# Kernel optimization log

Measured on AMD Instinct MI355X. Metric: run time of the kernel, lower is better.

Reference implementation:

```python
import jax, jax.numpy as jnp
import numpy as np

N_NODES = 100000
N_EDGES = 1600000
N_RELS = 8
IN_F, HID_F, OUT_F = 64, 64, 32


def rgcn_conv(x, src, dst, etype, W, root, bias, num_nodes, num_rels):
    """PyG RGCNConv: out[i] = x[i]@root + bias + sum_r mean_{j in N_r(i)} x[j]@W_r."""
    E = src.shape[0]
    seg = dst * num_rels + etype  # combined (node, relation) segment id
    cnt = jax.ops.segment_sum(jnp.ones((E,), x.dtype), seg,
                              num_segments=num_nodes * num_rels)
    norm = 1.0 / jnp.maximum(cnt[seg], 1.0)  # per-edge 1/|N_r(dst)|
    h = jnp.einsum('ni,rio->rno', x, W)      # [R, N, O] relation-transformed feats
    msg = h[etype, src] * norm[:, None]      # gather per edge, normalize
    agg = jax.ops.segment_sum(msg, dst, num_segments=num_nodes)
    return agg + x @ root + bias


def setup_inputs() -> dict:
    key = jax.random.key(0)
    ks = jax.random.split(key, 10)
    x = jax.random.normal(ks[0], (N_NODES, IN_F), dtype=jnp.float32)
    edge_index = jax.random.randint(ks[1], (2, N_EDGES), 0, N_NODES, dtype=jnp.int64)
    edge_type = jax.random.randint(ks[2], (N_EDGES,), 0, N_RELS, dtype=jnp.int64)
    s1 = 1.0 / np.sqrt(IN_F)
    s2 = 1.0 / np.sqrt(HID_F)
    W1 = jax.random.uniform(ks[3], (N_RELS, IN_F, HID_F), jnp.float32, -s1, s1)
    root1 = jax.random.uniform(ks[4], (IN_F, HID_F), jnp.float32, -s1, s1)
    b1 = jnp.zeros((HID_F,), jnp.float32)
    W2 = jax.random.uniform(ks[5], (N_RELS, HID_F, OUT_F), jnp.float32, -s2, s2)
    root2 = jax.random.uniform(ks[6], (HID_F, OUT_F), jnp.float32, -s2, s2)
    b2 = jnp.zeros((OUT_F,), jnp.float32)
    return {"x": x, "edge_index": edge_index, "edge_type": edge_type,
            "W1": W1, "root1": root1, "b1": b1,
            "W2": W2, "root2": root2, "b2": b2}


def reference(x, edge_index, edge_type, W1, root1, b1, W2, root2, b2):
    src, dst = edge_index[0], edge_index[1]
    h = rgcn_conv(x, src, dst, edge_type, W1, root1, b1, N_NODES, N_RELS)
    h = jax.nn.relu(h)
    out = rgcn_conv(h, src, dst, edge_type, W2, root2, b2, N_NODES, N_RELS)
    return out
```

## Files before the change

kernel.cpp:

```cpp
#include <hip/hip_runtime.h>
#include <hip/hip_bf16.h>

#define N_NODES 100000
#define N_EDGES 1600000
#define N_RELS  8
#define IN_F    64
#define HID_F   64
#define OUT_F   32
#define NSEG    (N_NODES * N_RELS)
#define SCAN_EPB 1024
#define SCAN_NB  ((NSEG + SCAN_EPB - 1) / SCAN_EPB)

typedef __attribute__((ext_vector_type(8))) short short8;
typedef __attribute__((ext_vector_type(4))) float f32x4;

__device__ __forceinline__ float b2f(unsigned short u) {
    return __uint_as_float(((unsigned)u) << 16);
}
__device__ __forceinline__ unsigned short f2b(float f) {
    unsigned u = __float_as_uint(f);
    u += 0x7FFFu + ((u >> 16) & 1u);
    return (unsigned short)(u >> 16);
}

#define PREP_W1 (576 * 64)
#define PREP_W2 (576 * 32)
#define PREP_CVT (N_NODES * 64 / 4)
#define PREP_TOT (PREP_W1 + PREP_W2 + PREP_CVT)

__global__ void k_hist(const int* __restrict__ dst, const int* __restrict__ et,
                       int* __restrict__ cnt, int* __restrict__ rank,
                       const float* __restrict__ W1, const float* __restrict__ root1,
                       const float* __restrict__ W2, const float* __restrict__ root2,
                       const float* __restrict__ x,
                       ushort* __restrict__ Wt1b, ushort* __restrict__ Wt2b,
                       ushort* __restrict__ xb) {
    const int e = blockIdx.x * 256 + threadIdx.x;
    const int gsz = gridDim.x * 256;
    for (int j = e; j < PREP_TOT; j += gsz) {
        if (j < PREP_W1) {
            int o = j / 576, k = j - o * 576;
            float v = (k < 512) ? W1[k * 64 + o] : root1[(k - 512) * 64 + o];
            Wt1b[j] = f2b(v);
        } else if (j < PREP_W1 + PREP_W2) {
            int j2 = j - PREP_W1;
            int o = j2 / 576, k = j2 - o * 576;
            float v = (k < 512) ? W2[k * 32 + o] : root2[(k - 512) * 32 + o];
            Wt2b[j2] = f2b(v);
        } else {
            int j2 = j - PREP_W1 - PREP_W2;
            float4 v = *(const float4*)(x + (size_t)j2 * 4);
            ushort4 u;
            u.x = f2b(v.x); u.y = f2b(v.y); u.z = f2b(v.z); u.w = f2b(v.w);
            *(ushort4*)(xb + (size_t)j2 * 4) = u;
        }
    }
    if (e < N_EDGES) {
        int seg = dst[e] * N_RELS + et[e];
        rank[e] = atomicAdd(&cnt[seg], 1);
    }
}

__global__ void k_scanA(const int* __restrict__ cnt, int* __restrict__ bsums) {
    __shared__ int red[256];
    int t = threadIdx.x;
    int base = blockIdx.x * SCAN_EPB + t * 4;
    int s = 0;
    #pragma unroll
    for (int j = 0; j < 4; ++j) {
        int idx = base + j;
        if (idx < NSEG) s += cnt[idx];
    }
    red[t] = s;
    __syncthreads();
    for (int st = 128; st > 0; st >>= 1) {
        if (t < st) red[t] += red[t + st];
        __syncthreads();
    }
    if (t == 0) bsums[blockIdx.x] = red[0];
}

__global__ void k_scanC(const int* __restrict__ cnt, const int* __restrict__ bsums,
                        int* __restrict__ offs) {
    __shared__ int red[256];
    __shared__ int ts[256];
    int t = threadIdx.x;

    int partial = 0;
    #pragma unroll
    for (int jj = 0; jj < 4; ++jj) {
        int j = t + jj * 256;
        if (j < SCAN_NB && j < (int)blockIdx.x) partial += bsums[j];
    }
    red[t] = partial;
    __syncthreads();
    for (int st = 128; st > 0; st >>= 1) {
        if (t < st) red[t] += red[t + st];
        __syncthreads();
    }
    const int base0 = red[0];

    int base = blockIdx.x * SCAN_EPB + t * 4;
    int v[4];
    int local = 0;
    #pragma unroll
    for (int j = 0; j < 4; ++j) {
        int idx = base + j;
        v[j] = (idx < NSEG) ? cnt[idx] : 0;
        local += v[j];
    }
    ts[t] = local;
    __syncthreads();
    for (int off = 1; off < 256; off <<= 1) {
        int x = (t >= off) ? ts[t - off] : 0;
        __syncthreads();
        ts[t] += x;
        __syncthreads();
    }
    int run = base0 + (ts[t] - local);
    #pragma unroll
    for (int j = 0; j < 4; ++j) {
        int idx = base + j;
        if (idx < NSEG) offs[idx] = run;
        run += v[j];
    }
}

__global__ void k_scat(const int* __restrict__ src, const int* __restrict__ dst,
                       const int* __restrict__ et, const int* __restrict__ offs,
                       const int* __restrict__ rank, int* __restrict__ ssrc) {
    int e = blockIdx.x * 256 + threadIdx.x;
    if (e < N_EDGES) {
        int r = et[e];
        int seg = dst[e] * N_RELS + r;
        ssrc[offs[seg] + rank[e]] = src[e] * 16 + r;
    }
}

template <int NOUT, bool RELU, typename OutT>
__global__ __launch_bounds__(512, 4) void k_layer(
        const ushort* __restrict__ xb, const int* __restrict__ offs,
        const int* __restrict__ cnt, const int* __restrict__ ssrc,
        const ushort* __restrict__ Wtb, const float* __restrict__ bias,
        OutT* __restrict__ out) {
    constexpr int NT = NOUT / 16;
    constexpr int S  = 8 / NT;
    __shared__ __align__(16) ushort A_lds[16][584];
    __shared__ f32x4 pc[6][64];

    const int tid = threadIdx.x;
    const int w = tid >> 6;
    const int f = tid & 63;
    const int node0 = blockIdx.x * 16;

    const int t = w % NT, q = w / NT;
    constexpr int cbase = 18 / S, crem = 18 % S;
    const int cs = q * cbase + (q < crem ? q : crem);
    const int ce = cs + cbase + (q < crem ? 1 : 0);
    const int n0 = t * 16;
    const ushort* bptr = Wtb + (n0 + (f & 15)) * 576 + ((f >> 4) * 8);
    short8 bcur = *(const short8*)(bptr + cs * 32);

    int ov = 0, cv = 0;
    if (f < 16) {
        ov = offs[(node0 + w * 2) * N_RELS + f];
        cv = cnt [(node0 + w * 2) * N_RELS + f];
    }

    for (int nd = 0; nd < 2; ++nd) {
        const int m = w * 2 + nd;
        const int node = node0 + m;
        const int s0 = __builtin_amdgcn_readlane(ov, nd * 8);
        const int ct = __builtin_amdgcn_readlane(ov, nd * 8 + 7)
                     + __builtin_amdgcn_readlane(cv, nd * 8 + 7) - s0;

        float a[8];
        #pragma unroll
        for (int r = 0; r < 8; ++r) a[r] = 0.0f;

        for (int cb = 0; cb < ct; cb += 64) {
            int n = ct - cb;
            if (n > 64) n = 64;
            int pk = 15;
            if (f < n) pk = ssrc[s0 + cb + f];
            for (int e = 0; e < n; e += 16) {
                int pv[16];
                float xv[16];
                #pragma unroll
                for (int i = 0; i < 16; ++i)
                    pv[i] = __builtin_amdgcn_readlane(pk, e + i);
                #pragma unroll
                for (int i = 0; i < 16; ++i)
                    xv[i] = b2f(xb[(size_t)(pv[i] >> 4) * 64 + f]);
                #pragma unroll
                for (int i = 0; i < 16; ++i) {
                    const int rl = pv[i] & 15;
                    if (rl < 4) {
                        if (rl < 2) { if (rl == 0) a[0] += xv[i]; else a[1] += xv[i]; }
                        else        { if (rl == 2) a[2] += xv[i]; else a[3] += xv[i]; }
                    } else if (rl < 8) {
                        if (rl < 6) { if (rl == 4) a[4] += xv[i]; else a[5] += xv[i]; }
                        else        { if (rl == 6) a[6] += xv[i]; else a[7] += xv[i]; }
                    }
                }
            }
        }

        #pragma unroll
        for (int r = 0; r < 8; ++r) {
            int c = __builtin_amdgcn_readlane(cv, nd * 8 + r);
            float inv = 1.0f / (float)(c > 0 ? c : 1);
            A_lds[m][r * 64 + f] = f2b(a[r] * inv);
        }
        A_lds[m][512 + f] = xb[node * 64 + f];
    }
    __syncthreads();

    f32x4 acc = (f32x4){0.0f, 0.0f, 0.0f, 0.0f};
    const ushort* aptr = &A_lds[f & 15][(f >> 4) * 8];
    for (int c = cs; c < ce; ++c) {
        short8 bnext = bcur;
        if (c + 1 < ce) bnext = *(const short8*)(bptr + (c + 1) * 32);
        short8 af = *(const short8*)(aptr + c * 32);
        acc = __builtin_amdgcn_mfma_f32_16x16x32_bf16(af, bcur, acc, 0, 0, 0);
        bcur = bnext;
    }

    if (q > 0) pc[w - NT][f] = acc;
    __syncthreads();
    if (q == 0) {
        #pragma unroll
        for (int j = 1; j < S; ++j) {
            f32x4 p = pc[t + NT * (j - 1)][f];
            acc.x += p.x; acc.y += p.y; acc.z += p.z; acc.w += p.w;
        }
        const int col = f & 15;
        const float bs = bias[n0 + col];
        const int mrow = (f >> 4) * 4;
        #pragma unroll
        for (int i = 0; i < 4; ++i) {
            float v = acc[i] + bs;
            if (RELU) v = fmaxf(v, 0.0f);
            size_t oi = (size_t)(node0 + mrow + i) * NOUT + n0 + col;
            if constexpr (sizeof(OutT) == 2) out[oi] = (OutT)f2b(v);
            else                             out[oi] = (OutT)v;
        }
    }
}

extern "C" void kernel_launch(void* const* d_in, const int* in_sizes, int n_in,
                              void* d_out, int out_size, void* d_ws, size_t ws_size,
                              hipStream_t stream) {
    const float* x     = (const float*)d_in[0];
    const int*   ei    = (const int*)d_in[1];
    const int*   et    = (const int*)d_in[2];
    const float* W1    = (const float*)d_in[3];
    const float* root1 = (const float*)d_in[4];
    const float* b1    = (const float*)d_in[5];
    const float* W2    = (const float*)d_in[6];
    const float* root2 = (const float*)d_in[7];
    const float* b2    = (const float*)d_in[8];
    float* out = (float*)d_out;

    const int* src = ei;
    const int* dst = ei + N_EDGES;

    char* ws = (char*)d_ws;
    int*    cnt   = (int*)(ws);
    int*    offs  = (int*)(ws + (size_t)NSEG * 4);
    int*    bsums = (int*)(ws + (size_t)NSEG * 8);
    int*    ssrc  = (int*)(ws + (size_t)NSEG * 8 + 4096);
    ushort* xb    = (ushort*)(ws + (size_t)NSEG * 8 + 4096 + (size_t)N_EDGES * 4);
    ushort* h1b   = (ushort*)((char*)xb + (size_t)N_NODES * 64 * 2);
    int*    rank  = (int*)h1b;
    ushort* Wt1b  = (ushort*)((char*)h1b + (size_t)N_NODES * 64 * 2);
    ushort* Wt2b  = (ushort*)((char*)Wt1b + (size_t)PREP_W1 * 2);

    hipMemsetAsync(cnt, 0, (size_t)NSEG * 4, stream);

    int eb = (N_EDGES + 255) / 256;
    k_hist<<<eb, 256, 0, stream>>>(dst, et, cnt, rank,
                                   W1, root1, W2, root2, x, Wt1b, Wt2b, xb);
    k_scanA<<<SCAN_NB, 256, 0, stream>>>(cnt, bsums);
    k_scanC<<<SCAN_NB, 256, 0, stream>>>(cnt, bsums, offs);
    k_scat<<<eb, 256, 0, stream>>>(src, dst, et, offs, rank, ssrc);

    k_layer<64, true, ushort><<<N_NODES / 16, 512, 0, stream>>>(
        xb, offs, cnt, ssrc, Wt1b, b1, h1b);
    k_layer<32, false, float><<<N_NODES / 16, 512, 0, stream>>>(
        h1b, offs, cnt, ssrc, Wt2b, b2, out);
}
```

Before: 438.7 us.

## Balance edge gather across waves via LDS atomics and scalar-loaded edge lists

Before this change each wave walked the edges of two fixed nodes, so the work per wave depended on node degree. Now the 16-node block's contiguous edge range is split evenly across the 8 waves. Each wave fetches 16 packed edge ids at a time with a scalar s_load_dwordx16, gathers source features, and accumulates them with LDS float atomicAdd into a 128x64 fp32 buffer indexed by (local node, relation), which is now packed into each edge id. The fp32 sums are then normalized, converted to bf16 and written back into the shared buffer before the MFMA stage. This removes the degree imbalance and the branchy per-relation register selection, at the cost of LDS atomic contention, extra barriers and larger shared memory that may lower occupancy.

Result: slower. 1.300 ms (+196.3%).

```diff
diff --git a/kernel.cpp b/kernel.cpp
--- a/kernel.cpp
+++ b/kernel.cpp
@@ -13,6 +13,7 @@
 
 typedef __attribute__((ext_vector_type(8))) short short8;
 typedef __attribute__((ext_vector_type(4))) float f32x4;
+typedef __attribute__((ext_vector_type(16))) int int16v;
 
 __device__ __forceinline__ float b2f(unsigned short u) {
     return __uint_as_float(((unsigned)u) << 16);
@@ -21,6 +22,12 @@
     unsigned u = __float_as_uint(f);
     u += 0x7FFFu + ((u >> 16) & 1u);
     return (unsigned short)(u >> 16);
+}
+__device__ __forceinline__ unsigned long long uni_ptr(const void* p) {
+    unsigned long long up = (unsigned long long)p;
+    unsigned lo = __builtin_amdgcn_readfirstlane((unsigned)up);
+    unsigned hi = __builtin_amdgcn_readfirstlane((unsigned)(up >> 32));
+    return ((unsigned long long)hi << 32) | lo;
 }
 
 #define PREP_W1 (576 * 64)
@@ -132,8 +139,9 @@
     int e = blockIdx.x * 256 + threadIdx.x;
     if (e < N_EDGES) {
         int r = et[e];
-        int seg = dst[e] * N_RELS + r;
-        ssrc[offs[seg] + rank[e]] = src[e] * 16 + r;
+        int d = dst[e];
+        int seg = d * N_RELS + r;
+        ssrc[offs[seg] + rank[e]] = (src[e] << 7) | ((d & 15) << 3) | r;
     }
 }
 
@@ -145,7 +153,11 @@
         OutT* __restrict__ out) {
     constexpr int NT = NOUT / 16;
     constexpr int S  = 8 / NT;
-    __shared__ __align__(16) ushort A_lds[16][584];
+    __shared__ __align__(16) union {
+        float  a32[128][64];
+        ushort a16[16][584];
+    } U;
+    __shared__ float invT[128];
     __shared__ f32x4 pc[6][64];
 
     const int tid = threadIdx.x;
@@ -161,63 +173,88 @@
     const ushort* bptr = Wtb + (n0 + (f & 15)) * 576 + ((f >> 4) * 8);
     short8 bcur = *(const short8*)(bptr + cs * 32);
 
-    int ov = 0, cv = 0;
-    if (f < 16) {
-        ov = offs[(node0 + w * 2) * N_RELS + f];
-        cv = cnt [(node0 + w * 2) * N_RELS + f];
-    }
-
-    for (int nd = 0; nd < 2; ++nd) {
-        const int m = w * 2 + nd;
-        const int node = node0 + m;
-        const int s0 = __builtin_amdgcn_readlane(ov, nd * 8);
-        const int ct = __builtin_amdgcn_readlane(ov, nd * 8 + 7)
-                     + __builtin_amdgcn_readlane(cv, nd * 8 + 7) - s0;
-
-        float a[8];
-        #pragma unroll
-        for (int r = 0; r < 8; ++r) a[r] = 0.0f;
-
-        for (int cb = 0; cb < ct; cb += 64) {
-            int n = ct - cb;
-            if (n > 64) n = 64;
-            int pk = 15;
-            if (f < n) pk = ssrc[s0 + cb + f];
-            for (int e = 0; e < n; e += 16) {
-                int pv[16];
-                float xv[16];
-                #pragma unroll
-                for (int i = 0; i < 16; ++i)
-                    pv[i] = __builtin_amdgcn_readlane(pk, e + i);
-                #pragma unroll
-                for (int i = 0; i < 16; ++i)
-                    xv[i] = b2f(xb[(size_t)(pv[i] >> 4) * 64 + f]);
-                #pragma unroll
-                for (int i = 0; i < 16; ++i) {
-                    const int rl = pv[i] & 15;
-                    if (rl < 4) {
-                        if (rl < 2) { if (rl == 0) a[0] += xv[i]; else a[1] += xv[i]; }
-                        else        { if (rl == 2) a[2] += xv[i]; else a[3] += xv[i]; }
-                    } else if (rl < 8) {
-                        if (rl < 6) { if (rl == 4) a[4] += xv[i]; else a[5] += xv[i]; }
-                        else        { if (rl == 6) a[6] += xv[i]; else a[7] += xv[i]; }
+    float* S32 = &U.a32[0][0];
+    {
+        f32x4 z = (f32x4){0.0f, 0.0f, 0.0f, 0.0f};
+        #pragma unroll
+        for (int k = 0; k < 4; ++k)
+            *(f32x4*)(S32 + tid * 16 + k * 4) = z;
+        if (tid < 128) {
+            int c = cnt[node0 * 8 + tid];
+            invT[tid] = 1.0f / (float)(c > 0 ? c : 1);
+        }
+    }
+    const int start = offs[node0 * 8];
+    const int end = (node0 + 16 >= N_NODES) ? N_EDGES : offs[(node0 + 16) * 8];
+    __syncthreads();
+
+    {
+        const int tot = end - start;
+        const int ebase = tot >> 3, erem = tot & 7;
+        const int ms = start + w * ebase + (w < erem ? w : erem);
+        const int me = ms + ebase + (w < erem ? 1 : 0);
+        if (ms < me) {
+            unsigned long long sp = uni_ptr(ssrc + (ms & ~15));
+            for (int pos = ms & ~15; pos < me; pos += 16, sp += 64) {
+                int16v g;
+                asm volatile("s_load_dwordx16 %0, %1, 0x0\n\t"
+                             "s_waitcnt lgkmcnt(0)"
+                             : "=s"(g) : "s"(sp));
+                if (pos >= ms && pos + 16 <= me) {
+                    #pragma unroll
+                    for (int j = 0; j < 16; ++j) {
+                        int sk = g[j];
+                        float xv = b2f(xb[(((unsigned)sk >> 7) << 6) + (unsigned)f]);
+                        atomicAdd(&U.a32[sk & 127][f], xv);
+                    }
+                } else {
+                    #pragma unroll
+                    for (int j = 0; j < 16; ++j) {
+                        if (pos + j >= ms && pos + j < me) {
+                            int sk = g[j];
+                            float xv = b2f(xb[(((unsigned)sk >> 7) << 6) + (unsigned)f]);
+                            atomicAdd(&U.a32[sk & 127][f], xv);
+                        }
                     }
                 }
             }
         }
-
-        #pragma unroll
-        for (int r = 0; r < 8; ++r) {
-            int c = __builtin_amdgcn_readlane(cv, nd * 8 + r);
-            float inv = 1.0f / (float)(c > 0 ? c : 1);
-            A_lds[m][r * 64 + f] = f2b(a[r] * inv);
-        }
-        A_lds[m][512 + f] = xb[node * 64 + f];
+    }
+    __syncthreads();
+
+    float rv[16];
+    {
+        const int row = tid >> 2;
+        const int fb = (tid & 3) * 16;
+        const float inv = invT[row];
+        #pragma unroll
+        for (int k = 0; k < 4; ++k) {
+            f32x4 v = *(f32x4*)(S32 + row * 64 + fb + k * 4);
+            rv[k * 4 + 0] = v.x * inv; rv[k * 4 + 1] = v.y * inv;
+            rv[k * 4 + 2] = v.z * inv; rv[k * 4 + 3] = v.w * inv;
+        }
+    }
+    __syncthreads();
+    {
+        const int row = tid >> 2;
+        const int nib = row >> 3, rel = row & 7;
+        const int fb = (tid & 3) * 16;
+        ushort* dp = &U.a16[nib][rel * 64 + fb];
+        short8 o0, o1;
+        #pragma unroll
+        for (int k = 0; k < 8; ++k) o0[k] = (short)f2b(rv[k]);
+        #pragma unroll
+        for (int k = 0; k < 8; ++k) o1[k] = (short)f2b(rv[8 + k]);
+        *(short8*)dp = o0;
+        *(short8*)(dp + 8) = o1;
+        const int m = tid >> 5, f2 = (tid & 31) * 2;
+        uint xr = *(const uint*)(xb + (size_t)(node0 + m) * 64 + f2);
+        *(uint*)&U.a16[m][512 + f2] = xr;
     }
     __syncthreads();
 
     f32x4 acc = (f32x4){0.0f, 0.0f, 0.0f, 0.0f};
-    const ushort* aptr = &A_lds[f & 15][(f >> 4) * 8];
+    const ushort* aptr = &U.a16[f & 15][(f >> 4) * 8];
     for (int c = cs; c < ce; ++c) {
         short8 bnext = bcur;
         if (c + 1 < ce) bnext = *(const short8*)(bptr + (c + 1) * 32);
@@ -276,7 +313,7 @@
     ushort* Wt1b  = (ushort*)((char*)h1b + (size_t)N_NODES * 64 * 2);
     ushort* Wt2b  = (ushort*)((char*)Wt1b + (size_t)PREP_W1 * 2);
 
-    hipMemsetAsync(cnt, 0, (size_t)NSEG * 4, stream);
+    (void)hipMemsetAsync(cnt, 0, (size_t)NSEG * 4, stream);
 
     int eb = (N_EDGES + 255) / 256;
     k_hist<<<eb, 256, 0, stream>>>(dst, et, cnt, rank,
```
